# Performance work log

Measured on AMD Instinct MI355X. Metric: run time of the kernel, lower is better.

Reference implementation:

```python
import jax, jax.numpy as jnp
import numpy as np

B, A_IN, C_IN, H, W_ = 8, 16, 4, 64, 64   # batch, input atoms, input capsules, spatial
K, C_OUT, A_OUT, ROUTINGS = 5, 8, 32, 3
EPS = 1e-7


def setup_inputs() -> dict:
    key = jax.random.key(0)
    k1, k2 = jax.random.split(key)
    x = jax.random.normal(k1, (B, A_IN, C_IN, H, W_), dtype=jnp.float32)
    # kaiming_uniform_(fan_in, relu): bound = sqrt(3) * sqrt(2) / sqrt(fan_in)
    fan_in = A_IN * K * K
    bound = float(np.sqrt(6.0 / fan_in))
    W = jax.random.uniform(k2, (C_OUT * A_OUT, A_IN, K, K), jnp.float32, -bound, bound)
    b = jnp.full((1, 1, C_OUT, A_OUT), 0.1, dtype=jnp.float32)
    return {"x": x, "W": W, "b": b}


def _squash(v):
    # v: (..., atoms); SegCaps squash with epsilon inside sqrt
    sq = jnp.sum(v * v, axis=-1, keepdims=True)
    return v * (sq / (1.0 + sq) / jnp.sqrt(sq + EPS))


def reference(x, W, b):
    # Faithful to torch: permute then raw row-major reshapes (byte reinterpret)
    t = jnp.transpose(x, (2, 0, 3, 4, 1))                      # (C_IN, B, H, W, A_IN)
    t = t.reshape(C_IN * B, H, W_, A_IN).reshape(-1, A_IN, H, W_)
    conv = jax.lax.conv_general_dilated(
        t, W, window_strides=(1, 1), padding="SAME",
        dimension_numbers=("NCHW", "OIHW", "NCHW"))             # (C_IN*B, C_OUT*A_OUT, h, w)
    ch, cw = conv.shape[2], conv.shape[3]
    votes = conv.reshape(B, C_IN, ch, cw, C_OUT, A_OUT)         # raw reinterpret, as in torch
    biases = jnp.tile(b, (ch, cw, 1, 1))                        # (h, w, C_OUT, A_OUT)

    # dynamic routing (SegCaps update_routing)
    logits = jnp.zeros((B, C_IN, ch, cw, C_OUT), dtype=votes.dtype)
    activation = None
    for _ in range(ROUTINGS):
        route = jax.nn.softmax(logits, axis=-1)                 # (B, Cin, h, w, Cout)
        preact = jnp.einsum("bihwo,bihwoa->bhwoa", route, votes) + biases
        activation = _squash(preact)                            # (B, h, w, Cout, A)
        agreement = jnp.einsum("bihwoa,bhwoa->bihwo", votes, activation)
        logits = logits + agreement
    return jnp.transpose(activation, (0, 4, 3, 1, 2))           # (B, A_OUT, C_OUT, h, w)
```

## Files before the change

kernel.cpp:

```cpp
#include <hip/hip_runtime.h>
#include <hip/hip_bf16.h>


typedef _Float16 half8 __attribute__((ext_vector_type(8)));
typedef _Float16 half4v __attribute__((ext_vector_type(4)));
typedef float floatx4 __attribute__((ext_vector_type(4)));

#define EPSF 1e-7f


__global__ __launch_bounds__(256) void k_prep(const float* __restrict__ x,
                                              const float* __restrict__ W,
                                              _Float16* __restrict__ thp,
                                              _Float16* __restrict__ Wp) {
  const int tid = threadIdx.x;
  if (blockIdx.x < 256) {
    __shared__ float lin[32 * 306 + 18];
    const int bid = blockIdx.x;
    const int n   = bid >> 3;
    const int a0h = (bid >> 2) & 1;
    const int W0  = (bid & 3) * 16;
    const int ci = n >> 3, b0 = n & 7;
    const float* xb = x + b0 * 262144 + ci * 4096 + W0;
    for (int p = 0; p < 8; ++p) {
      int rr = p * 64 + (tid >> 2);
      int qq = (tid & 3) * 4;
      int a1 = rr >> 5, m = rr & 31;
      float4 v = *(const float4*)(xb + a1 * 16384 + (a0h * 32 + m) * 64 + qq);
      float* d = lin + m * 306 + a1 * 18 + qq;
      d[0] = v.x; d[1] = v.y; d[2] = v.z; d[3] = v.w;
    }
    __syncthreads();
    for (int hh = 0; hh < 4; ++hh) {
      int w1 = tid >> 4, a1 = tid & 15;
      int h = hh * 16 + ((W0 + w1) >> 2);
      int w = ((W0 + w1) & 3) * 16 + a1;
      half8 v;
#pragma unroll
      for (int j = 0; j < 8; ++j)
        v[j] = (_Float16)lin[(j * 4 + hh) * 306 + a1 * 18 + w1];
      size_t chunk = ((size_t)(n * 2 + a0h) * 68 + (h + 2)) * 68 + (w + 2);
      *(half8*)(thp + chunk * 8) = v;
    }
  } else {
    int id = (blockIdx.x - 256) * 256 + tid;
    int a  = id & 15;
    int oc = (id >> 4) & 255;
    int kk = id >> 12;
    Wp[id] = (kk < 25) ? (_Float16)W[oc * 400 + a * 25 + kk] : (_Float16)0.0f;
  }
}

__global__ __launch_bounds__(256) void k_conv(
    const _Float16* __restrict__ thp, const _Float16* __restrict__ Wp,
    _Float16* __restrict__ votes) {
  __shared__ _Float16 slab[5440];
  const int y = blockIdx.x;
  const int n = blockIdx.y;
  const int tid = threadIdx.x;

  const size_t base0 = (size_t)(n * 2) * 36992 + (size_t)y * 544;
  for (int c = tid; c < 680; c += 256) {
    int ah  = (c >= 340);
    int rem = c - ah * 340;
    *(half8*)(slab + c * 8) =
        *(const half8*)(thp + base0 + (size_t)ah * 36992 + rem * 8);
  }

  const int lane  = tid & 63;
  const int wv    = tid >> 6;
  const int col16 = lane & 15;
  const int quad  = lane >> 4;
  const int t     = quad >> 1;
  const int a0h   = quad & 1;
  const int m0    = wv * 64;

  floatx4 acc[4][4] = {};

  const _Float16* wb = Wp + (size_t)t * 4096 + (m0 + col16) * 16 + a0h * 8;
  half8 wf[4], wf1[4], wf2[4], pf[4], pf1[4];
#pragma unroll
  for (int oct = 0; oct < 4; ++oct) {
    wf[oct]  = *(const half8*)(wb + oct * 256);
    wf1[oct] = *(const half8*)(wb + 8192 + oct * 256);
  }

  __syncthreads();

#pragma unroll
  for (int xt = 0; xt < 4; ++xt)
    pf[xt] = *(const half8*)(slab + (a0h * 340 + xt * 16 + col16 + t) * 8);

  for (int s = 0; s < 13; ++s) {
    int s2 = (s + 2 < 13) ? s + 2 : 12;
#pragma unroll
    for (int oct = 0; oct < 4; ++oct)
      wf2[oct] = *(const half8*)(wb + (size_t)s2 * 8192 + oct * 256);
    int kkb1 = 2 * (s + 1) + t; if (kkb1 > 24) kkb1 = 24;
    int ky1 = kkb1 / 5, kx1 = kkb1 - ky1 * 5;
    const _Float16* lb1 = slab + (a0h * 340 + ky1 * 68 + col16 + kx1) * 8;
#pragma unroll
    for (int xt = 0; xt < 4; ++xt)
      pf1[xt] = *(const half8*)(lb1 + xt * 128);
#pragma unroll
    for (int xt = 0; xt < 4; ++xt)
#pragma unroll
      for (int oct = 0; oct < 4; ++oct)
        acc[xt][oct] = __builtin_amdgcn_mfma_f32_16x16x32_f16(
            pf[xt], wf[oct], acc[xt][oct], 0, 0, 0);
#pragma unroll
    for (int oct = 0; oct < 4; ++oct) { wf[oct] = wf1[oct]; wf1[oct] = wf2[oct]; }
#pragma unroll
    for (int xt = 0; xt < 4; ++xt) pf[xt] = pf1[xt];
  }

  _Float16* vbase = votes + (size_t)n * 1048576 + y * 64;
#pragma unroll
  for (int oct = 0; oct < 4; ++oct) {
    int oc = m0 + oct * 16 + col16;
#pragma unroll
    for (int xt = 0; xt < 4; ++xt) {
      half4v o4;
      o4.x = (_Float16)acc[xt][oct][0];
      o4.y = (_Float16)acc[xt][oct][1];
      o4.z = (_Float16)acc[xt][oct][2];
      o4.w = (_Float16)acc[xt][oct][3];
      *(half4v*)(vbase + (size_t)oc * 4096 + xt * 16 + quad * 4) = o4;
    }
  }
}

__global__ __launch_bounds__(256) void k_routing4(
    const _Float16* __restrict__ votes, const float* __restrict__ bias,
    float* __restrict__ out) {
  __shared__ float so[256 * 17];
  const int tid  = threadIdx.x;
  const int lane = tid & 63;
  const int wv   = tid >> 6;
  const int bid  = blockIdx.x;
  const int bv = bid >> 8;
  const int h  = (bid >> 2) & 63;
  const int W0 = (bid & 3) * 16;

  float4 bia = *(const float4*)(bias + lane * 4);
  const int o = lane >> 3;
  const int m = lane & 7;

  float act[4][4];

  const _Float16* vb0 = votes + (size_t)bv * 4194304 + h * 16384
                        + (W0 + wv * 4) * 256 + lane * 4;

#pragma unroll
  for (int k = 0; k < 4; ++k) {
    float4 v[4];
#pragma unroll
    for (int i = 0; i < 4; ++i) {
      half4v hv = *(const half4v*)(vb0 + k * 256 + (size_t)i * 1048576);
      v[i] = make_float4((float)hv.x, (float)hv.y, (float)hv.z, (float)hv.w);
    }

    float pr[4] = {bia.x, bia.y, bia.z, bia.w};
#pragma unroll
    for (int i = 0; i < 4; ++i) {
      pr[0] = fmaf(0.125f, v[i].x, pr[0]);
      pr[1] = fmaf(0.125f, v[i].y, pr[1]);
      pr[2] = fmaf(0.125f, v[i].z, pr[2]);
      pr[3] = fmaf(0.125f, v[i].w, pr[3]);
    }
    float sq = pr[0]*pr[0] + pr[1]*pr[1] + pr[2]*pr[2] + pr[3]*pr[3];
    sq += __shfl_xor(sq, 1, 64);
    sq += __shfl_xor(sq, 2, 64);
    sq += __shfl_xor(sq, 4, 64);
    float scale = sq / (1.f + sq) / sqrtf(sq + EPSF);
    float a0 = pr[0]*scale, a1 = pr[1]*scale, a2 = pr[2]*scale, a3 = pr[3]*scale;

    float logit[4];
#pragma unroll
    for (int i = 0; i < 4; ++i) {
      float ag = v[i].x*a0 + v[i].y*a1 + v[i].z*a2 + v[i].w*a3;
      ag += __shfl_xor(ag, 1, 64);
      ag += __shfl_xor(ag, 2, 64);
      ag += __shfl_xor(ag, 4, 64);
      logit[i] = ag;
    }

#pragma unroll
    for (int r = 1; r < 3; ++r) {
      float route[4];
#pragma unroll
      for (int i = 0; i < 4; ++i) {
        float e = __expf(logit[i]);
        float s = e;
        s += __shfl_xor(s, 8, 64);
        s += __shfl_xor(s, 16, 64);
        s += __shfl_xor(s, 32, 64);
        route[i] = e / s;
      }
      pr[0] = bia.x; pr[1] = bia.y; pr[2] = bia.z; pr[3] = bia.w;
#pragma unroll
      for (int i = 0; i < 4; ++i) {
        pr[0] = fmaf(route[i], v[i].x, pr[0]);
        pr[1] = fmaf(route[i], v[i].y, pr[1]);
        pr[2] = fmaf(route[i], v[i].z, pr[2]);
        pr[3] = fmaf(route[i], v[i].w, pr[3]);
      }
      sq = pr[0]*pr[0] + pr[1]*pr[1] + pr[2]*pr[2] + pr[3]*pr[3];
      sq += __shfl_xor(sq, 1, 64);
      sq += __shfl_xor(sq, 2, 64);
      sq += __shfl_xor(sq, 4, 64);
      scale = sq / (1.f + sq) / sqrtf(sq + EPSF);
      a0 = pr[0]*scale; a1 = pr[1]*scale; a2 = pr[2]*scale; a3 = pr[3]*scale;

      if (r == 1) {
#pragma unroll
        for (int i = 0; i < 4; ++i) {
          float ag = v[i].x*a0 + v[i].y*a1 + v[i].z*a2 + v[i].w*a3;
          ag += __shfl_xor(ag, 1, 64);
          ag += __shfl_xor(ag, 2, 64);
          ag += __shfl_xor(ag, 4, 64);
          logit[i] += ag;
        }
      }
    }
    act[k][0] = a0; act[k][1] = a1; act[k][2] = a2; act[k][3] = a3;
  }

#pragma unroll
  for (int k = 0; k < 4; ++k)
#pragma unroll
    for (int j = 0; j < 4; ++j)
      so[((m * 4 + j) * 8 + o) * 17 + wv * 4 + k] = act[k][j];
  __syncthreads();

  float* ob = out + (size_t)bv * 1048576 + h * 64 + W0;
  for (int p = 0; p < 4; ++p) {
    int rg = p * 64 + (tid >> 2);
    int w0 = (tid & 3) * 4;
    const float* sp = so + rg * 17 + w0;
    float4 val = make_float4(sp[0], sp[1], sp[2], sp[3]);
    *(float4*)(ob + (size_t)rg * 4096 + w0) = val;
  }
}

extern "C" void kernel_launch(void* const* d_in, const int* in_sizes, int n_in,
                              void* d_out, int out_size, void* d_ws, size_t ws_size,
                              hipStream_t stream) {
  const float* x  = (const float*)d_in[0];
  const float* W  = (const float*)d_in[1];
  const float* b  = (const float*)d_in[2];
  float* out = (float*)d_out;

  _Float16* thp   = (_Float16*)d_ws;
  _Float16* Wp    = thp + 2367488;
  _Float16* votes = Wp + 106496;

  hipMemsetAsync(thp, 0, 2367488 * sizeof(_Float16), stream);
  k_prep<<<672, 256, 0, stream>>>(x, W, thp, Wp);
  k_conv<<<dim3(64, 32), 256, 0, stream>>>(thp, Wp, votes);
  k_routing4<<<2048, 256, 0, stream>>>(votes, b, out);
}
```

Measured before the change: 144.6 us.

## Fuse input transpose and padding into conv slab load, drop memset and prep pass

```diff
diff --git a/kernel.cpp b/kernel.cpp
--- a/kernel.cpp
+++ b/kernel.cpp
@@ -8,64 +8,57 @@
 
 #define EPSF 1e-7f
 
-
-__global__ __launch_bounds__(256) void k_prep(const float* __restrict__ x,
-                                              const float* __restrict__ W,
-                                              _Float16* __restrict__ thp,
-                                              _Float16* __restrict__ Wp) {
-  const int tid = threadIdx.x;
-  if (blockIdx.x < 256) {
-    __shared__ float lin[32 * 306 + 18];
-    const int bid = blockIdx.x;
-    const int n   = bid >> 3;
-    const int a0h = (bid >> 2) & 1;
-    const int W0  = (bid & 3) * 16;
-    const int ci = n >> 3, b0 = n & 7;
-    const float* xb = x + b0 * 262144 + ci * 4096 + W0;
-    for (int p = 0; p < 8; ++p) {
-      int rr = p * 64 + (tid >> 2);
-      int qq = (tid & 3) * 4;
-      int a1 = rr >> 5, m = rr & 31;
-      float4 v = *(const float4*)(xb + a1 * 16384 + (a0h * 32 + m) * 64 + qq);
-      float* d = lin + m * 306 + a1 * 18 + qq;
-      d[0] = v.x; d[1] = v.y; d[2] = v.z; d[3] = v.w;
-    }
-    __syncthreads();
-    for (int hh = 0; hh < 4; ++hh) {
-      int w1 = tid >> 4, a1 = tid & 15;
-      int h = hh * 16 + ((W0 + w1) >> 2);
-      int w = ((W0 + w1) & 3) * 16 + a1;
-      half8 v;
-#pragma unroll
-      for (int j = 0; j < 8; ++j)
-        v[j] = (_Float16)lin[(j * 4 + hh) * 306 + a1 * 18 + w1];
-      size_t chunk = ((size_t)(n * 2 + a0h) * 68 + (h + 2)) * 68 + (w + 2);
-      *(half8*)(thp + chunk * 8) = v;
-    }
-  } else {
-    int id = (blockIdx.x - 256) * 256 + tid;
-    int a  = id & 15;
-    int oc = (id >> 4) & 255;
-    int kk = id >> 12;
-    Wp[id] = (kk < 25) ? (_Float16)W[oc * 400 + a * 25 + kk] : (_Float16)0.0f;
-  }
+__global__ __launch_bounds__(256) void k_packw(const float* __restrict__ W,
+                                               _Float16* __restrict__ Wp) {
+  int id = blockIdx.x * 256 + threadIdx.x;
+  int a  = id & 15;
+  int oc = (id >> 4) & 255;
+  int kk = id >> 12;
+  Wp[id] = (kk < 25) ? (_Float16)W[oc * 400 + a * 25 + kk] : (_Float16)0.0f;
 }
 
 __global__ __launch_bounds__(256) void k_conv(
-    const _Float16* __restrict__ thp, const _Float16* __restrict__ Wp,
+    const float* __restrict__ x, const _Float16* __restrict__ Wp,
     _Float16* __restrict__ votes) {
   __shared__ _Float16 slab[5440];
   const int y = blockIdx.x;
   const int n = blockIdx.y;
   const int tid = threadIdx.x;
-
-  const size_t base0 = (size_t)(n * 2) * 36992 + (size_t)y * 544;
-  for (int c = tid; c < 680; c += 256) {
-    int ah  = (c >= 340);
-    int rem = c - ah * 340;
-    *(half8*)(slab + c * 8) =
-        *(const half8*)(thp + base0 + (size_t)ah * 36992 + rem * 8);
-  }
+  const int ci = n >> 3, b0 = n & 7;
+  const float* xb = x + b0 * 262144 + ci * 4096;
+
+  for (int c = tid; c < 1280; c += 256) {
+    int a   = c / 80;
+    int rem = c - a * 80;
+    int rr  = rem >> 4;
+    int a1  = rem & 15;
+    int h   = y + rr - 2;
+    int ah  = a >> 3, sub = a & 7;
+    _Float16* sb = slab + ((ah * 5 + rr) * 68 + a1 + 2) * 8 + sub;
+    if (h >= 0 && h < 64) {
+      float4 v = *(const float4*)(xb + a1 * 16384
+                                  + (a * 4 + (h >> 4)) * 64 + (h & 15) * 4);
+      sb[0 * 128]  = (_Float16)v.x;
+      sb[16 * 8]   = (_Float16)v.y;
+      sb[32 * 8]   = (_Float16)v.z;
+      sb[48 * 8]   = (_Float16)v.w;
+    } else {
+      sb[0 * 128]  = (_Float16)0.0f;
+      sb[16 * 8]   = (_Float16)0.0f;
+      sb[32 * 8]   = (_Float16)0.0f;
+      sb[48 * 8]   = (_Float16)0.0f;
+    }
+  }
+  if (tid < 40) {
+    int ah  = tid / 20;
+    int rem = tid - ah * 20;
+    int rr  = rem >> 2;
+    int hci = rem & 3;
+    int hc  = (hci < 2) ? hci : (64 + hci);
+    half8 z = {};
+    *(half8*)(slab + ((ah * 5 + rr) * 68 + hc) * 8) = z;
+  }
+  __syncthreads();
 
   const int lane  = tid & 63;
   const int wv    = tid >> 6;
@@ -84,8 +77,6 @@
     wf[oct]  = *(const half8*)(wb + oct * 256);
     wf1[oct] = *(const half8*)(wb + 8192 + oct * 256);
   }
-
-  __syncthreads();
 
 #pragma unroll
   for (int xt = 0; xt < 4; ++xt)
@@ -251,12 +242,10 @@
   const float* b  = (const float*)d_in[2];
   float* out = (float*)d_out;
 
-  _Float16* thp   = (_Float16*)d_ws;
-  _Float16* Wp    = thp + 2367488;
+  _Float16* Wp    = (_Float16*)d_ws;
   _Float16* votes = Wp + 106496;
 
-  hipMemsetAsync(thp, 0, 2367488 * sizeof(_Float16), stream);
-  k_prep<<<672, 256, 0, stream>>>(x, W, thp, Wp);
-  k_conv<<<dim3(64, 32), 256, 0, stream>>>(thp, Wp, votes);
+  k_packw<<<416, 256, 0, stream>>>(W, Wp);
+  k_conv<<<dim3(64, 32), 256, 0, stream>>>(x, Wp, votes);
   k_routing4<<<2048, 256, 0, stream>>>(votes, b, out);
 }
```

After: 149.9 us. 1.04x slower.
